# Kernel tuning notes

Hardware: AMD Instinct MI355X
Metric: run time of the kernel (lower is better)

## Reference

```python
import jax, jax.numpy as jnp
import numpy as np

H = 64
NG = 100000   # gene nodes
ND = 30000    # disease nodes
NE = 1500000  # gda edges (gene -> disease)
NL = 500000   # supervision (label) edges


def setup_inputs() -> dict:
    key = jax.random.key(0)
    ks = jax.random.split(key, 20)
    s = 0.1
    inp = {
        "gene_emb":    jax.random.normal(ks[0], (NG, H), jnp.float32) * s,
        "disease_emb": jax.random.normal(ks[1], (ND, H), jnp.float32) * s,
    }
    wnames = ["w1_gd_l", "w1_gd_r", "w1_dg_l", "w1_dg_r",
              "w2_gd_l", "w2_gd_r", "w2_dg_l", "w2_dg_r"]
    for i, n in enumerate(wnames):
        inp[n] = jax.random.normal(ks[2 + i], (H, H), jnp.float32) * s
    for i, n in enumerate(["b1_gd", "b1_dg", "b2_gd", "b2_dg"]):
        inp[n] = jax.random.normal(ks[10 + i], (H,), jnp.float32) * 0.01
    inp["edge_src"]  = jax.random.randint(ks[14], (NE,), 0, NG)
    inp["edge_dst"]  = jax.random.randint(ks[15], (NE,), 0, ND)
    inp["label_src"] = jax.random.randint(ks[16], (NL,), 0, NG)
    inp["label_dst"] = jax.random.randint(ks[17], (NL,), 0, ND)
    return inp


def _sage(x_src, x_dst, src, dst, n_dst, wl, wr, b):
    # SAGEConv (mean aggr): lin_l(mean_{j in N(i)} x_j) + lin_r(x_i) + b
    msum = jax.ops.segment_sum(x_src[src], dst, num_segments=n_dst)
    cnt = jax.ops.segment_sum(jnp.ones((src.shape[0], 1), x_src.dtype), dst,
                              num_segments=n_dst)
    mean = msum / jnp.maximum(cnt, 1.0)
    return mean @ wl + x_dst @ wr + b


def reference(gene_emb, disease_emb,
              w1_gd_l, w1_gd_r, b1_gd, w1_dg_l, w1_dg_r, b1_dg,
              w2_gd_l, w2_gd_r, b2_gd, w2_dg_l, w2_dg_r, b2_dg,
              edge_src, edge_dst, label_src, label_dst):
    # layer 1 (hetero: gene->disease via gda, disease->gene via rev_gda)
    h_d = jax.nn.relu(_sage(gene_emb, disease_emb, edge_src, edge_dst, ND,
                            w1_gd_l, w1_gd_r, b1_gd))
    h_g = jax.nn.relu(_sage(disease_emb, gene_emb, edge_dst, edge_src, NG,
                            w1_dg_l, w1_dg_r, b1_dg))
    # layer 2 (no activation)
    h_d2 = _sage(h_g, h_d, edge_src, edge_dst, ND, w2_gd_l, w2_gd_r, b2_gd)
    h_g2 = _sage(h_d, h_g, edge_dst, edge_src, NG, w2_dg_l, w2_dg_r, b2_dg)
    # classifier: dot product over label edges
    return jnp.sum(h_g2[label_src] * h_d2[label_dst], axis=-1)
```

## Files before the change

kernel.cpp:

```cpp
#include <hip/hip_runtime.h>
#include <hip/hip_bf16.h>

#define H 64
#define SCAN_CHUNK 512
#define NB1 512

typedef unsigned short u16;
typedef unsigned int u32;
typedef unsigned char u8;
typedef __attribute__((ext_vector_type(8))) __bf16 bf16x8;
typedef __attribute__((ext_vector_type(4))) float f32x4;
typedef __attribute__((ext_vector_type(2))) float f32x2;

__device__ __forceinline__ float bflo(u32 u) {
    return __builtin_bit_cast(float, u << 16);
}
__device__ __forceinline__ float bfhi(u32 u) {
    return __builtin_bit_cast(float, u & 0xffff0000u);
}
__device__ __forceinline__ u16 bf16rne(float f) {
    u32 u = __builtin_bit_cast(u32, f);
    return (u16)((u + 0x7FFFu + ((u >> 16) & 1u)) >> 16);
}
__device__ __forceinline__ u8 fp8enc(float f) {
    return (u8)(__builtin_amdgcn_cvt_pk_fp8_f32(f, 0.0f, 0, false) & 0xFF);
}

__global__ __launch_bounds__(256) void fused_count_convert_kernel(
    const int* __restrict__ es, const int* __restrict__ ed,
    int* __restrict__ histD, int* __restrict__ histG,
    int ne, int shiftD, int shiftG,
    const float* __restrict__ a, u16* __restrict__ oa, u32* __restrict__ oa8,
    long long na4,
    const float* __restrict__ b, u16* __restrict__ ob, u32* __restrict__ ob8,
    long long nb4)
{
    if (blockIdx.x < NB1) {
        __shared__ int lhd[256], lhg[256];
        const int tid = threadIdx.x;
        lhd[tid] = 0; lhg[tid] = 0;
        __syncthreads();
        const int chunk = (ne + NB1 - 1) / NB1;
        const int e0 = blockIdx.x * chunk;
        const int e1 = min(e0 + chunk, ne);
        for (int e = e0 + tid; e < e1; e += 256) {
            atomicAdd(&lhd[ed[e] >> shiftD], 1);
            atomicAdd(&lhg[es[e] >> shiftG], 1);
        }
        __syncthreads();
        histD[tid * NB1 + blockIdx.x] = lhd[tid];
        histG[tid * NB1 + blockIdx.x] = lhg[tid];
        return;
    }
    long long i = (long long)(blockIdx.x - NB1) * 256 + threadIdx.x;
    const float* src; u16* dst; u32* dst8; long long q;
    if (i < na4) { src = a; dst = oa; dst8 = oa8; q = i; }
    else if (i < na4 + nb4) { src = b; dst = ob; dst8 = ob8; q = i - na4; }
    else return;
    float4 v = *(const float4*)&src[q * 4];
    ushort4 o;
    o.x = bf16rne(v.x); o.y = bf16rne(v.y);
    o.z = bf16rne(v.z); o.w = bf16rne(v.w);
    *(ushort4*)&dst[q * 4] = o;
    int r = 0;
    r = __builtin_amdgcn_cvt_pk_fp8_f32(v.x * 16.0f, v.y * 16.0f, r, false);
    r = __builtin_amdgcn_cvt_pk_fp8_f32(v.z * 16.0f, v.w * 16.0f, r, true);
    dst8[q] = (u32)r;
}

__global__ __launch_bounds__(256) void scan_reduce_kernel(
    const int* __restrict__ a1, int n1, const int* __restrict__ a2, int n2,
    int B1, int* __restrict__ partial,
    u32* __restrict__ pad0, u32* __restrict__ pad1,
    u32* __restrict__ pad2, u32* __restrict__ pad3)
{
    if (blockIdx.x == 0) {
        int tz = threadIdx.x;
        if (tz < 16) pad0[tz] = 0;
        else if (tz < 32) pad1[tz - 16] = 0;
        else if (tz < 48) pad2[tz - 32] = 0;
        else if (tz < 64) pad3[tz - 48] = 0;
    }
    const int b = blockIdx.x;
    const int* a; int n, base;
    if (b < B1) { a = a1; n = n1; base = b * SCAN_CHUNK; }
    else        { a = a2; n = n2; base = (b - B1) * SCAN_CHUNK; }
    int t = threadIdx.x;
    int i0 = base + 2 * t, i1 = i0 + 1;
    int v = ((i0 < n) ? a[i0] : 0) + ((i1 < n) ? a[i1] : 0);
    #pragma unroll
    for (int off = 32; off > 0; off >>= 1) v += __shfl_down(v, off, 64);
    __shared__ int ws[4];
    if ((t & 63) == 0) ws[t >> 6] = v;
    __syncthreads();
    if (t == 0) partial[b] = ws[0] + ws[1] + ws[2] + ws[3];
}

__global__ __launch_bounds__(256) void scan_apply_kernel(
    const int* __restrict__ a1, int* __restrict__ out1, int n1,
    const int* __restrict__ a2, int* __restrict__ out2, int n2,
    int B1, int nbtot, const int* __restrict__ partial)
{
    __shared__ int sExcl[1024];
    __shared__ int ws[4];
    const int tid = threadIdx.x;
    const int lane = tid & 63, wid = tid >> 6;

    int j0 = 4 * tid;
    int p0 = (j0 + 0 < nbtot) ? partial[j0 + 0] : 0;
    int p1 = (j0 + 1 < nbtot) ? partial[j0 + 1] : 0;
    int p2 = (j0 + 2 < nbtot) ? partial[j0 + 2] : 0;
    int p3 = (j0 + 3 < nbtot) ? partial[j0 + 3] : 0;
    int psum = p0 + p1 + p2 + p3;
    int P = psum;
    #pragma unroll
    for (int off = 1; off < 64; off <<= 1) {
        int u = __shfl_up(P, off, 64);
        if (lane >= off) P += u;
    }
    if (lane == 63) ws[wid] = P;
    __syncthreads();
    int wbase = 0;
    #pragma unroll
    for (int w = 0; w < 4; ++w) wbase += (w < wid) ? ws[w] : 0;
    int e = wbase + (P - psum);
    sExcl[j0 + 0] = e;
    sExcl[j0 + 1] = e + p0;
    sExcl[j0 + 2] = e + p0 + p1;
    sExcl[j0 + 3] = e + p0 + p1 + p2;
    __syncthreads();

    const int b = blockIdx.x;
    int tot1 = sExcl[B1 - 1] + partial[B1 - 1];
    int myOff = sExcl[b] - ((b >= B1) ? tot1 : 0);
    if (b == 0 && tid == 0) {
        int tot2 = sExcl[nbtot - 1] + partial[nbtot - 1] - tot1;
        out1[n1] = tot1;
        out2[n2] = tot2;
    }
    __syncthreads();

    const int* a; int* out; int n, base;
    if (b < B1) { a = a1; out = out1; n = n1; base = b * SCAN_CHUNK; }
    else        { a = a2; out = out2; n = n2; base = (b - B1) * SCAN_CHUNK; }
    int i0 = base + 2 * tid, i1 = i0 + 1;
    int x0 = (i0 < n) ? a[i0] : 0;
    int x1 = (i1 < n) ? a[i1] : 0;
    int p = x0 + x1;
    int Q = p;
    #pragma unroll
    for (int off = 1; off < 64; off <<= 1) {
        int u = __shfl_up(Q, off, 64);
        if (lane >= off) Q += u;
    }
    if (lane == 63) ws[wid] = Q;
    __syncthreads();
    int waveBase = 0;
    #pragma unroll
    for (int w = 0; w < 4; ++w) waveBase += (w < wid) ? ws[w] : 0;
    int off0 = myOff + waveBase + (Q - p);
    if (i0 < n) out[i0] = off0;
    if (i1 < n) out[i1] = off0 + x0;
}

__global__ __launch_bounds__(256) void part_scatter_kernel(
    const int* __restrict__ es, const int* __restrict__ ed,
    const int* __restrict__ baseD, const int* __restrict__ baseG,
    u32* __restrict__ pairD, u32* __restrict__ pairG,
    int ne, int shiftD, int shiftG)
{
    __shared__ int curD[256], curG[256];
    const int tid = threadIdx.x;
    curD[tid] = baseD[tid * NB1 + blockIdx.x];
    curG[tid] = baseG[tid * NB1 + blockIdx.x];
    __syncthreads();
    const int maskD = (1 << shiftD) - 1;
    const int maskG = (1 << shiftG) - 1;
    const int chunk = (ne + NB1 - 1) / NB1;
    const int e0 = blockIdx.x * chunk;
    const int e1 = min(e0 + chunk, ne);
    for (int e = e0 + tid; e < e1; e += 256) {
        int s = es[e], d = ed[e];
        int pD = atomicAdd(&curD[d >> shiftD], 1);
        pairD[pD] = ((u32)(d & maskD) << 17) | (u32)s;
        int pG = atomicAdd(&curG[s >> shiftG], 1);
        pairG[pG] = ((u32)(s & maskG) << 17) | (u32)d;
    }
}

__global__ __launch_bounds__(256) void csr_build_kernel(
    const u32* __restrict__ pairD, const int* __restrict__ baseD,
    int* __restrict__ rowD, int* __restrict__ idxD, int nd, int shiftD, int nbktD,
    const u32* __restrict__ pairG, const int* __restrict__ baseG,
    int* __restrict__ rowG, int* __restrict__ idxG, int ng, int shiftG, int nbktG)
{
    __shared__ int lcnt[512], lcur[512];
    __shared__ int ws[4];
    const int j = blockIdx.x & 255;
    const int isG = blockIdx.x >> 8;
    const u32* pair; const int* base; int* row; int* idx; int n, shift, nbkt;
    if (isG) { pair = pairG; base = baseG; row = rowG; idx = idxG; n = ng; shift = shiftG; nbkt = nbktG; }
    else     { pair = pairD; base = baseD; row = rowD; idx = idxD; n = nd; shift = shiftD; nbkt = nbktD; }
    if (j >= nbkt) return;

    const int tid = threadIdx.x;
    const int nLo = j << shift;
    const int nHi = min(nLo + (1 << shift), n);
    const int range = nHi - nLo;
    const int segBase = base[j * NB1];
    const int segEnd  = base[(j + 1) * NB1];

    lcnt[tid] = 0; lcnt[tid + 256] = 0;
    __syncthreads();
    for (int t = segBase + tid; t < segEnd; t += 256)
        atomicAdd(&lcnt[pair[t] >> 17], 1);
    __syncthreads();

    int i0 = 2 * tid, i1 = i0 + 1;
    int c0 = (i0 < range) ? lcnt[i0] : 0;
    int c1 = (i1 < range) ? lcnt[i1] : 0;
    int p = c0 + c1;
    int P = p;
    const int lane = tid & 63, wid = tid >> 6;
    #pragma unroll
    for (int off = 1; off < 64; off <<= 1) {
        int u = __shfl_up(P, off, 64);
        if (lane >= off) P += u;
    }
    if (lane == 63) ws[wid] = P;
    __syncthreads();
    int waveBase = 0;
    #pragma unroll
    for (int w = 0; w < 4; ++w) waveBase += (w < wid) ? ws[w] : 0;
    int o0 = segBase + waveBase + (P - p);
    int o1 = o0 + c0;
    if (i0 < range) { row[nLo + i0] = o0; lcur[i0] = o0; }
    if (i1 < range) { row[nLo + i1] = o1; lcur[i1] = o1; }
    if (nHi == n && tid == 0) row[n] = segEnd;
    __syncthreads();

    for (int t = segBase + tid; t < segEnd; t += 256) {
        u32 pr = pair[t];
        int pos = atomicAdd(&lcur[pr >> 17], 1);
        idx[pos] = (int)(pr & 0x1FFFFu);
    }
}

__global__ __launch_bounds__(256) void gather_mean_kernel(
    const u8* __restrict__ srcD, const u8* __restrict__ srcG,
    const int* __restrict__ rowD, const int* __restrict__ idxD,
    const int* __restrict__ rowG, const int* __restrict__ idxG,
    u16* __restrict__ outD, u16* __restrict__ outG, int nd, int ng)
{
    int hw = blockIdx.x * 8 + (threadIdx.x >> 5);
    int l5 = threadIdx.x & 31;
    if (hw >= nd + ng) return;
    const bool isD = hw < nd;
    const int sub = l5 >> 3;
    const int c8 = l5 & 7;
    const u8* src; const int* row; const int* idx; u16* out; int node, npad;
    if (isD) { src = srcD; row = rowD; idx = idxD; out = outD; node = hw;      npad = ng; }
    else     { src = srcG; row = rowG; idx = idxG; out = outG; node = hw - nd; npad = nd; }
    int beg = row[node], end = row[node + 1];
    const u8* srcc = src + c8 * 8;

    f32x2 aA[4], aB[4];
    #pragma unroll
    for (int j = 0; j < 4; ++j) {
        aA[j] = (f32x2){0.f, 0.f}; aB[j] = (f32x2){0.f, 0.f};
    }

    for (int i = beg; i < end; i += 32) {
        int p = i + sub;
        const int* ip = idx + p;
        int t0 = ip[0],  t1 = ip[4],  t2 = ip[8],  t3 = ip[12];
        int t4 = ip[16], t5 = ip[20], t6 = ip[24], t7 = ip[28];
        int s0 = (p      < end) ? t0 : npad;
        int s1 = (p + 4  < end) ? t1 : npad;
        int s2 = (p + 8  < end) ? t2 : npad;
        int s3 = (p + 12 < end) ? t3 : npad;
        int s4 = (p + 16 < end) ? t4 : npad;
        int s5 = (p + 20 < end) ? t5 : npad;
        int s6 = (p + 24 < end) ? t6 : npad;
        int s7 = (p + 28 < end) ? t7 : npad;
        uint2 v0 = *(const uint2*)(srcc + (size_t)s0 * 64);
        uint2 v1 = *(const uint2*)(srcc + (size_t)s1 * 64);
        uint2 v2 = *(const uint2*)(srcc + (size_t)s2 * 64);
        uint2 v3 = *(const uint2*)(srcc + (size_t)s3 * 64);
        uint2 v4 = *(const uint2*)(srcc + (size_t)s4 * 64);
        uint2 v5 = *(const uint2*)(srcc + (size_t)s5 * 64);
        uint2 v6 = *(const uint2*)(srcc + (size_t)s6 * 64);
        uint2 v7 = *(const uint2*)(srcc + (size_t)s7 * 64);
        aA[0] += __builtin_amdgcn_cvt_pk_f32_fp8((int)v0.x, false);
        aA[1] += __builtin_amdgcn_cvt_pk_f32_fp8((int)v0.x, true);
        aA[2] += __builtin_amdgcn_cvt_pk_f32_fp8((int)v0.y, false);
        aA[3] += __builtin_amdgcn_cvt_pk_f32_fp8((int)v0.y, true);
        aA[0] += __builtin_amdgcn_cvt_pk_f32_fp8((int)v1.x, false);
        aA[1] += __builtin_amdgcn_cvt_pk_f32_fp8((int)v1.x, true);
        aA[2] += __builtin_amdgcn_cvt_pk_f32_fp8((int)v1.y, false);
        aA[3] += __builtin_amdgcn_cvt_pk_f32_fp8((int)v1.y, true);
        aA[0] += __builtin_amdgcn_cvt_pk_f32_fp8((int)v2.x, false);
        aA[1] += __builtin_amdgcn_cvt_pk_f32_fp8((int)v2.x, true);
        aA[2] += __builtin_amdgcn_cvt_pk_f32_fp8((int)v2.y, false);
        aA[3] += __builtin_amdgcn_cvt_pk_f32_fp8((int)v2.y, true);
        aA[0] += __builtin_amdgcn_cvt_pk_f32_fp8((int)v3.x, false);
        aA[1] += __builtin_amdgcn_cvt_pk_f32_fp8((int)v3.x, true);
        aA[2] += __builtin_amdgcn_cvt_pk_f32_fp8((int)v3.y, false);
        aA[3] += __builtin_amdgcn_cvt_pk_f32_fp8((int)v3.y, true);
        aB[0] += __builtin_amdgcn_cvt_pk_f32_fp8((int)v4.x, false);
        aB[1] += __builtin_amdgcn_cvt_pk_f32_fp8((int)v4.x, true);
        aB[2] += __builtin_amdgcn_cvt_pk_f32_fp8((int)v4.y, false);
        aB[3] += __builtin_amdgcn_cvt_pk_f32_fp8((int)v4.y, true);
        aB[0] += __builtin_amdgcn_cvt_pk_f32_fp8((int)v5.x, false);
        aB[1] += __builtin_amdgcn_cvt_pk_f32_fp8((int)v5.x, true);
        aB[2] += __builtin_amdgcn_cvt_pk_f32_fp8((int)v5.y, false);
        aB[3] += __builtin_amdgcn_cvt_pk_f32_fp8((int)v5.y, true);
        aB[0] += __builtin_amdgcn_cvt_pk_f32_fp8((int)v6.x, false);
        aB[1] += __builtin_amdgcn_cvt_pk_f32_fp8((int)v6.x, true);
        aB[2] += __builtin_amdgcn_cvt_pk_f32_fp8((int)v6.y, false);
        aB[3] += __builtin_amdgcn_cvt_pk_f32_fp8((int)v6.y, true);
        aB[0] += __builtin_amdgcn_cvt_pk_f32_fp8((int)v7.x, false);
        aB[1] += __builtin_amdgcn_cvt_pk_f32_fp8((int)v7.x, true);
        aB[2] += __builtin_amdgcn_cvt_pk_f32_fp8((int)v7.y, false);
        aB[3] += __builtin_amdgcn_cvt_pk_f32_fp8((int)v7.y, true);
    }

    f32x2 acc[4];
    #pragma unroll
    for (int j = 0; j < 4; ++j) acc[j] = aA[j] + aB[j];
    #pragma unroll
    for (int j = 0; j < 4; ++j) {
        f32x2 t;
        t.x = __shfl_xor(acc[j].x, 8, 64);
        t.y = __shfl_xor(acc[j].y, 8, 64);
        acc[j] += t;
        t.x = __shfl_xor(acc[j].x, 16, 64);
        t.y = __shfl_xor(acc[j].y, 16, 64);
        acc[j] += t;
    }
    if (sub == 0) {
        float inv = 0.0625f / fmaxf((float)(end - beg), 1.0f);
        u32 w0 = (u32)bf16rne(acc[0].x * inv) | ((u32)bf16rne(acc[0].y * inv) << 16);
        u32 w1 = (u32)bf16rne(acc[1].x * inv) | ((u32)bf16rne(acc[1].y * inv) << 16);
        u32 w2 = (u32)bf16rne(acc[2].x * inv) | ((u32)bf16rne(acc[2].y * inv) << 16);
        u32 w3 = (u32)bf16rne(acc[3].x * inv) | ((u32)bf16rne(acc[3].y * inv) << 16);
        uint4 pk = make_uint4(w0, w1, w2, w3);
        *(uint4*)(out + (size_t)node * H + c8 * 8) = pk;
    }
}

template <bool RELU, bool F8OUT>
__global__ __launch_bounds__(256) void sage_mm_mfma_kernel(
    const u16* __restrict__ meanD, const u16* __restrict__ xD, u16* __restrict__ outD,
    u8* __restrict__ outDf8,
    const float* __restrict__ wlD, const float* __restrict__ wrD,
    const float* __restrict__ bD, int nd,
    const u16* __restrict__ meanG, const u16* __restrict__ xG, u16* __restrict__ outG,
    u8* __restrict__ outGf8,
    const float* __restrict__ wlG, const float* __restrict__ wrG,
    const float* __restrict__ bG, int ng, int MBD)
{
    __shared__ u16 sB[16 * 64 * 8];
    int b = blockIdx.x;
    const u16 *mean, *x; u16* out; u8* out8; const float *wl, *wr, *bias; int n;
    if (b < MBD) { mean = meanD; x = xD; out = outD; out8 = outDf8; wl = wlD; wr = wrD; bias = bD; n = nd; }
    else { b -= MBD; mean = meanG; x = xG; out = outG; out8 = outGf8; wl = wlG; wr = wrG; bias = bG; n = ng; }

    const int tid = threadIdx.x;
    for (int i = tid; i < 4096; i += 256) {
        int k = i >> 6, ncol = i & 63;
        int q = (k >> 3) & 3, j = k & 7, t = ncol >> 4, n15 = ncol & 15;
        int lane = q * 16 + n15;
        int c0 = k >> 5;
        sB[(((c0 + 0) * 4 + t) * 64 + lane) * 8 + j] = bf16rne(wl[i]);
        sB[(((c0 + 2) * 4 + t) * 64 + lane) * 8 + j] = bf16rne(wr[i]);
    }
    __syncthreads();

    const int lane = tid & 63;
    const int wave = tid >> 6;
    const int m = lane & 15;
    const int q = lane >> 4;

    bf16x8 Bf[16];
    {
        const uint4* sB4 = (const uint4*)sB;
        #pragma unroll
        for (int f = 0; f < 16; ++f)
            Bf[f] = __builtin_bit_cast(bf16x8, sB4[f * 64 + lane]);
    }
    float bv[4];
    #pragma unroll
    for (int t = 0; t < 4; ++t) bv[t] = bias[t * 16 + m];

    const int row0 = b * 256;
    #pragma unroll
    for (int r = 0; r < 4; ++r) {
        int rbase = row0 + (wave + 4 * r) * 16;
        if (rbase >= n) break;
        int gr = min(rbase + m, n - 1);
        const uint4* mrow = (const uint4*)(mean + (size_t)gr * H);
        const uint4* xrow = (const uint4*)(x + (size_t)gr * H);
        bf16x8 A0 = __builtin_bit_cast(bf16x8, mrow[q]);
        bf16x8 A1 = __builtin_bit_cast(bf16x8, mrow[q + 4]);
        bf16x8 A2 = __builtin_bit_cast(bf16x8, xrow[q]);
        bf16x8 A3 = __builtin_bit_cast(bf16x8, xrow[q + 4]);
        f32x4 acc[4];
        #pragma unroll
        for (int t = 0; t < 4; ++t) acc[t] = (f32x4){bv[t], bv[t], bv[t], bv[t]};
        #pragma unroll
        for (int t = 0; t < 4; ++t) {
            acc[t] = __builtin_amdgcn_mfma_f32_16x16x32_bf16(A0, Bf[0 * 4 + t], acc[t], 0, 0, 0);
            acc[t] = __builtin_amdgcn_mfma_f32_16x16x32_bf16(A1, Bf[1 * 4 + t], acc[t], 0, 0, 0);
            acc[t] = __builtin_amdgcn_mfma_f32_16x16x32_bf16(A2, Bf[2 * 4 + t], acc[t], 0, 0, 0);
            acc[t] = __builtin_amdgcn_mfma_f32_16x16x32_bf16(A3, Bf[3 * 4 + t], acc[t], 0, 0, 0);
        }
        #pragma unroll
        for (int reg = 0; reg < 4; ++reg) {
            int orow = rbase + q * 4 + reg;
            if (orow < n) {
                u16* op = out + (size_t)orow * H;
                u8* op8 = F8OUT ? (out8 + (size_t)orow * H) : nullptr;
                #pragma unroll
                for (int t = 0; t < 4; ++t) {
                    float v = acc[t][reg];
                    if (RELU) v = fmaxf(v, 0.0f);
                    op[t * 16 + m] = bf16rne(v);
                    if (F8OUT) op8[t * 16 + m] = fp8enc(v * 16.0f);
                }
            }
        }
    }
}

__global__ __launch_bounds__(256) void classify_kernel(
    const u16* __restrict__ hg2, const u16* __restrict__ hd2,
    const int* __restrict__ ls, const int* __restrict__ ld,
    float* __restrict__ out, int nl)
{
    long long t = (long long)blockIdx.x * blockDim.x + threadIdx.x;
    int e = (int)(t >> 3);
    int c8 = (int)(t & 7);
    if (e >= nl) return;
    int a = ls[e];
    int b = ld[e];
    uint4 ua = *((const uint4*)(hg2 + (size_t)a * H) + c8);
    uint4 ub = *((const uint4*)(hd2 + (size_t)b * H) + c8);
    float v = bflo(ua.x) * bflo(ub.x) + bfhi(ua.x) * bfhi(ub.x)
            + bflo(ua.y) * bflo(ub.y) + bfhi(ua.y) * bfhi(ub.y)
            + bflo(ua.z) * bflo(ub.z) + bfhi(ua.z) * bfhi(ub.z)
            + bflo(ua.w) * bflo(ub.w) + bfhi(ua.w) * bfhi(ub.w);
    v += __shfl_xor(v, 1, 64);
    v += __shfl_xor(v, 2, 64);
    v += __shfl_xor(v, 4, 64);
    if (c8 == 0) out[e] = v;
}

extern "C" void kernel_launch(void* const* d_in, const int* in_sizes, int n_in,
                              void* d_out, int out_size, void* d_ws, size_t ws_size,
                              hipStream_t stream)
{
    const float* gene  = (const float*)d_in[0];
    const float* dis   = (const float*)d_in[1];
    const float* w1gdl = (const float*)d_in[2];
    const float* w1gdr = (const float*)d_in[3];
    const float* w1dgl = (const float*)d_in[4];
    const float* w1dgr = (const float*)d_in[5];
    const float* w2gdl = (const float*)d_in[6];
    const float* w2gdr = (const float*)d_in[7];
    const float* w2dgl = (const float*)d_in[8];
    const float* w2dgr = (const float*)d_in[9];
    const float* b1gd  = (const float*)d_in[10];
    const float* b1dg  = (const float*)d_in[11];
    const float* b2gd  = (const float*)d_in[12];
    const float* b2dg  = (const float*)d_in[13];
    const int* es = (const int*)d_in[14];
    const int* ed = (const int*)d_in[15];
    const int* ls = (const int*)d_in[16];
    const int* ld = (const int*)d_in[17];

    const int ng = in_sizes[0] / H;
    const int nd = in_sizes[1] / H;
    const int ne = in_sizes[14];
    const int nl = in_sizes[16];

    int shiftD = 0; while (((nd + (1 << shiftD) - 1) >> shiftD) > 256) ++shiftD;
    int shiftG = 0; while (((ng + (1 << shiftG) - 1) >> shiftG) > 256) ++shiftG;
    const int nbktD = (nd + (1 << shiftD) - 1) >> shiftD;
    const int nbktG = (ng + (1 << shiftG) - 1) >> shiftG;
    const int n1 = 256 * NB1;

    int* rowD = (int*)d_ws;
    int* rowG = rowD + nd + 1;
    int* idxD = rowG + ng + 1;
    int* idxG = idxD + ne;
    u16* geneBf = (u16*)(idxG + ne);
    u16* disBf  = geneBf + (size_t)ng * H;
    u16* h1Dbf  = disBf + (size_t)nd * H;
    u16* h1Gbf  = h1Dbf + (size_t)nd * H;
    u16* h2Dbf  = h1Gbf + (size_t)ng * H;
    u16* h2Gbf  = h2Dbf + (size_t)nd * H;
    uintptr_t pf8 = (uintptr_t)(h2Gbf + (size_t)ng * H);
    pf8 = (pf8 + 15) & ~(uintptr_t)15;
    u32* geneF8 = (u32*)pf8;
    u32* disF8  = geneF8 + (size_t)ng * 16 + 16;
    u32* h1DF8  = disF8 + (size_t)nd * 16 + 16;
    u32* h1GF8  = h1DF8 + (size_t)nd * 16 + 16;
    uintptr_t p = (uintptr_t)(h1GF8 + (size_t)ng * 16 + 16);
    p = (p + 15) & ~(uintptr_t)15;
    u16* MD = (u16*)p;
    u16* MG = MD + (size_t)nd * H;
    int* histD = (int*)p;
    int* histG = histD + n1;
    int* baseD = histG + n1;
    int* baseG = baseD + n1 + 1;
    int* partial  = baseG + n1 + 1;
    uintptr_t pp = (uintptr_t)(partial + 1024);
    pp = (pp + 15) & ~(uintptr_t)15;
    u32* pairD = (u32*)pp;
    u32* pairG = pairD + ne;

    const long long na4 = (long long)ng * H / 4;
    const long long nb4 = (long long)nd * H / 4;
    const int convBlocks = (int)((na4 + nb4 + 255) / 256);
    fused_count_convert_kernel<<<NB1 + convBlocks, 256, 0, stream>>>(
        es, ed, histD, histG, ne, shiftD, shiftG,
        gene, geneBf, geneF8, na4, dis, disBf, disF8, nb4);

    const int B1 = n1 / SCAN_CHUNK;
    const int nbtot = 2 * B1;
    scan_reduce_kernel<<<nbtot, 256, 0, stream>>>(histD, n1, histG, n1, B1, partial,
                                                  geneF8 + (size_t)ng * 16,
                                                  disF8 + (size_t)nd * 16,
                                                  h1DF8 + (size_t)nd * 16,
                                                  h1GF8 + (size_t)ng * 16);
    scan_apply_kernel<<<nbtot, 256, 0, stream>>>(histD, baseD, n1,
                                                 histG, baseG, n1, B1, nbtot, partial);

    part_scatter_kernel<<<NB1, 256, 0, stream>>>(es, ed, baseD, baseG,
                                                 pairD, pairG, ne, shiftD, shiftG);
    csr_build_kernel<<<512, 256, 0, stream>>>(
        pairD, baseD, rowD, idxD, nd, shiftD, nbktD,
        pairG, baseG, rowG, idxG, ng, shiftG, nbktG);

    const int gatherBlocks = (nd + ng + 7) / 8;
    const int MBD = (nd + 255) / 256;
    const int MBG = (ng + 255) / 256;

    gather_mean_kernel<<<gatherBlocks, 256, 0, stream>>>(
        (const u8*)geneF8, (const u8*)disF8, rowD, idxD, rowG, idxG, MD, MG, nd, ng);
    sage_mm_mfma_kernel<true, true><<<MBD + MBG, 256, 0, stream>>>(
        MD, disBf, h1Dbf, (u8*)h1DF8, w1gdl, w1gdr, b1gd, nd,
        MG, geneBf, h1Gbf, (u8*)h1GF8, w1dgl, w1dgr, b1dg, ng, MBD);

    gather_mean_kernel<<<gatherBlocks, 256, 0, stream>>>(
        (const u8*)h1GF8, (const u8*)h1DF8, rowD, idxD, rowG, idxG, MD, MG, nd, ng);
    sage_mm_mfma_kernel<false, false><<<MBD + MBG, 256, 0, stream>>>(
        MD, h1Dbf, h2Dbf, nullptr, w2gdl, w2gdr, b2gd, nd,
        MG, h1Gbf, h2Gbf, nullptr, w2dgl, w2dgr, b2dg, ng, MBD);

    {
        long long threads = (long long)nl * 8;
        int blocks = (int)((threads + 255) / 256);
        classify_kernel<<<blocks, 256, 0, stream>>>(h2Gbf, h2Dbf, ls, ld,
                                                    (float*)d_out, nl);
    }
}
```

Before: 317.4 us.

## Sub-bucket disease CSR by gene-index range to improve gather locality

The CSR build for disease nodes now splits each node's neighbour list into four sub-segments keyed by the high bits of the gene index (idx>>15), so consecutive gathers in a segment touch a narrower band of the gene feature table. The gather kernel walks the four sub-segments per disease node. Index loads and output stores are switched to nontemporal hints. The intent is better cache locality on the random source-row gathers, at the cost of more row-pointer storage, a larger per-bucket histogram and extra loop overhead for partially filled sub-segments.

```diff
diff --git a/kernel.cpp b/kernel.cpp
--- a/kernel.cpp
+++ b/kernel.cpp
@@ -11,6 +11,7 @@
 typedef __attribute__((ext_vector_type(8))) __bf16 bf16x8;
 typedef __attribute__((ext_vector_type(4))) float f32x4;
 typedef __attribute__((ext_vector_type(2))) float f32x2;
+typedef __attribute__((ext_vector_type(4))) u32 u32x4;
 
 __device__ __forceinline__ float bflo(u32 u) {
     return __builtin_bit_cast(float, u << 16);
@@ -212,13 +213,21 @@
 
     lcnt[tid] = 0; lcnt[tid + 256] = 0;
     __syncthreads();
-    for (int t = segBase + tid; t < segEnd; t += 256)
-        atomicAdd(&lcnt[pair[t] >> 17], 1);
-    __syncthreads();
-
+    if (isG) {
+        for (int t = segBase + tid; t < segEnd; t += 256)
+            atomicAdd(&lcnt[pair[t] >> 17], 1);
+    } else {
+        for (int t = segBase + tid; t < segEnd; t += 256) {
+            u32 pr = pair[t];
+            atomicAdd(&lcnt[((pr >> 17) << 2) | ((pr & 0x1FFFFu) >> 15)], 1);
+        }
+    }
+    __syncthreads();
+
+    const int elems = isG ? range : (range << 2);
     int i0 = 2 * tid, i1 = i0 + 1;
-    int c0 = (i0 < range) ? lcnt[i0] : 0;
-    int c1 = (i1 < range) ? lcnt[i1] : 0;
+    int c0 = (i0 < elems) ? lcnt[i0] : 0;
+    int c1 = (i1 < elems) ? lcnt[i1] : 0;
     int p = c0 + c1;
     int P = p;
     const int lane = tid & 63, wid = tid >> 6;
@@ -234,47 +243,42 @@
     for (int w = 0; w < 4; ++w) waveBase += (w < wid) ? ws[w] : 0;
     int o0 = segBase + waveBase + (P - p);
     int o1 = o0 + c0;
-    if (i0 < range) { row[nLo + i0] = o0; lcur[i0] = o0; }
-    if (i1 < range) { row[nLo + i1] = o1; lcur[i1] = o1; }
-    if (nHi == n && tid == 0) row[n] = segEnd;
-    __syncthreads();
-
-    for (int t = segBase + tid; t < segEnd; t += 256) {
-        u32 pr = pair[t];
-        int pos = atomicAdd(&lcur[pr >> 17], 1);
-        idx[pos] = (int)(pr & 0x1FFFFu);
-    }
-}
-
-__global__ __launch_bounds__(256) void gather_mean_kernel(
-    const u8* __restrict__ srcD, const u8* __restrict__ srcG,
-    const int* __restrict__ rowD, const int* __restrict__ idxD,
-    const int* __restrict__ rowG, const int* __restrict__ idxG,
-    u16* __restrict__ outD, u16* __restrict__ outG, int nd, int ng)
-{
-    int hw = blockIdx.x * 8 + (threadIdx.x >> 5);
-    int l5 = threadIdx.x & 31;
-    if (hw >= nd + ng) return;
-    const bool isD = hw < nd;
-    const int sub = l5 >> 3;
-    const int c8 = l5 & 7;
-    const u8* src; const int* row; const int* idx; u16* out; int node, npad;
-    if (isD) { src = srcD; row = rowD; idx = idxD; out = outD; node = hw;      npad = ng; }
-    else     { src = srcG; row = rowG; idx = idxG; out = outG; node = hw - nd; npad = nd; }
-    int beg = row[node], end = row[node + 1];
-    const u8* srcc = src + c8 * 8;
-
-    f32x2 aA[4], aB[4];
-    #pragma unroll
-    for (int j = 0; j < 4; ++j) {
-        aA[j] = (f32x2){0.f, 0.f}; aB[j] = (f32x2){0.f, 0.f};
-    }
-
+    int* rowOut = row + (isG ? nLo : (nLo << 2));
+    if (i0 < elems) { rowOut[i0] = o0; lcur[i0] = o0; }
+    if (i1 < elems) { rowOut[i1] = o1; lcur[i1] = o1; }
+    if (nHi == n && tid == 0) row[isG ? n : (n << 2)] = segEnd;
+    __syncthreads();
+
+    if (isG) {
+        for (int t = segBase + tid; t < segEnd; t += 256) {
+            u32 pr = pair[t];
+            int pos = atomicAdd(&lcur[pr >> 17], 1);
+            idx[pos] = (int)(pr & 0x1FFFFu);
+        }
+    } else {
+        for (int t = segBase + tid; t < segEnd; t += 256) {
+            u32 pr = pair[t];
+            int pos = atomicAdd(&lcur[((pr >> 17) << 2) | ((pr & 0x1FFFFu) >> 15)], 1);
+            idx[pos] = (int)(pr & 0x1FFFFu);
+        }
+    }
+}
+
+__device__ __forceinline__ void gather_seg(
+    const int* __restrict__ idx, const u8* __restrict__ srcc,
+    int beg, int end, int npad, int sub, f32x2* aA, f32x2* aB)
+{
     for (int i = beg; i < end; i += 32) {
         int p = i + sub;
         const int* ip = idx + p;
-        int t0 = ip[0],  t1 = ip[4],  t2 = ip[8],  t3 = ip[12];
-        int t4 = ip[16], t5 = ip[20], t6 = ip[24], t7 = ip[28];
+        int t0 = __builtin_nontemporal_load(ip +  0);
+        int t1 = __builtin_nontemporal_load(ip +  4);
+        int t2 = __builtin_nontemporal_load(ip +  8);
+        int t3 = __builtin_nontemporal_load(ip + 12);
+        int t4 = __builtin_nontemporal_load(ip + 16);
+        int t5 = __builtin_nontemporal_load(ip + 20);
+        int t6 = __builtin_nontemporal_load(ip + 24);
+        int t7 = __builtin_nontemporal_load(ip + 28);
         int s0 = (p      < end) ? t0 : npad;
         int s1 = (p + 4  < end) ? t1 : npad;
         int s2 = (p + 8  < end) ? t2 : npad;
@@ -324,6 +328,45 @@
         aB[2] += __builtin_amdgcn_cvt_pk_f32_fp8((int)v7.y, false);
         aB[3] += __builtin_amdgcn_cvt_pk_f32_fp8((int)v7.y, true);
     }
+}
+
+__global__ __launch_bounds__(256) void gather_mean_kernel(
+    const u8* __restrict__ srcD, const u8* __restrict__ srcG,
+    const int* __restrict__ rowD2, const int* __restrict__ idxD,
+    const int* __restrict__ rowG, const int* __restrict__ idxG,
+    u16* __restrict__ outD, u16* __restrict__ outG, int nd, int ng)
+{
+    int hw = blockIdx.x * 8 + (threadIdx.x >> 5);
+    int l5 = threadIdx.x & 31;
+    if (hw >= nd + ng) return;
+    const bool isD = hw < nd;
+    const int sub = l5 >> 3;
+    const int c8 = l5 & 7;
+
+    f32x2 aA[4], aB[4];
+    #pragma unroll
+    for (int j = 0; j < 4; ++j) {
+        aA[j] = (f32x2){0.f, 0.f}; aB[j] = (f32x2){0.f, 0.f};
+    }
+
+    int deg;
+    if (isD) {
+        const u8* srcc = srcD + c8 * 8;
+        int rb = hw << 2;
+        int b0 = rowD2[rb], b1 = rowD2[rb + 1], b2 = rowD2[rb + 2];
+        int b3 = rowD2[rb + 3], b4 = rowD2[rb + 4];
+        deg = b4 - b0;
+        gather_seg(idxD, srcc, b0, b1, ng, sub, aA, aB);
+        gather_seg(idxD, srcc, b1, b2, ng, sub, aA, aB);
+        gather_seg(idxD, srcc, b2, b3, ng, sub, aA, aB);
+        gather_seg(idxD, srcc, b3, b4, ng, sub, aA, aB);
+    } else {
+        const u8* srcc = srcG + c8 * 8;
+        int node = hw - nd;
+        int beg = rowG[node], end = rowG[node + 1];
+        deg = end - beg;
+        gather_seg(idxG, srcc, beg, end, nd, sub, aA, aB);
+    }
 
     f32x2 acc[4];
     #pragma unroll
@@ -339,13 +382,15 @@
         acc[j] += t;
     }
     if (sub == 0) {
-        float inv = 0.0625f / fmaxf((float)(end - beg), 1.0f);
-        u32 w0 = (u32)bf16rne(acc[0].x * inv) | ((u32)bf16rne(acc[0].y * inv) << 16);
-        u32 w1 = (u32)bf16rne(acc[1].x * inv) | ((u32)bf16rne(acc[1].y * inv) << 16);
-        u32 w2 = (u32)bf16rne(acc[2].x * inv) | ((u32)bf16rne(acc[2].y * inv) << 16);
-        u32 w3 = (u32)bf16rne(acc[3].x * inv) | ((u32)bf16rne(acc[3].y * inv) << 16);
-        uint4 pk = make_uint4(w0, w1, w2, w3);
-        *(uint4*)(out + (size_t)node * H + c8 * 8) = pk;
+        u16* out = isD ? outD : outG;
+        int node = isD ? hw : hw - nd;
+        float inv = 0.0625f / fmaxf((float)deg, 1.0f);
+        u32x4 pk;
+        pk.x = (u32)bf16rne(acc[0].x * inv) | ((u32)bf16rne(acc[0].y * inv) << 16);
+        pk.y = (u32)bf16rne(acc[1].x * inv) | ((u32)bf16rne(acc[1].y * inv) << 16);
+        pk.z = (u32)bf16rne(acc[2].x * inv) | ((u32)bf16rne(acc[2].y * inv) << 16);
+        pk.w = (u32)bf16rne(acc[3].x * inv) | ((u32)bf16rne(acc[3].y * inv) << 16);
+        __builtin_nontemporal_store(pk, (u32x4*)(out + (size_t)node * H + c8 * 8));
     }
 }
 
@@ -491,7 +536,7 @@
     const int n1 = 256 * NB1;
 
     int* rowD = (int*)d_ws;
-    int* rowG = rowD + nd + 1;
+    int* rowG = rowD + nd * 4 + 1;
     int* idxD = rowG + ng + 1;
     int* idxG = idxD + ne;
     u16* geneBf = (u16*)(idxG + ne);
```

Result: slower. 348.1 us (+9.7%).

## Fuse neighbor mean gather with MFMA SAGE linear into one kernel

Applied to the files above, without the earlier changes.

Merges the gather-mean kernel and the MFMA matmul kernel so each 256-thread block gathers 32 nodes' neighbor means into shared memory (XOR-swizzled) and then runs the linear layers on them with MFMA. This removes the global write and re-read of the bf16 mean buffers and one launch per layer. In exchange, every block reloads and reformats the full weight matrices into shared memory for only 32 rows, and the MFMA phase now uses only two 16-row groups split across waves, so the per-row matmul overhead rises.

```diff
diff --git a/kernel.cpp b/kernel.cpp
--- a/kernel.cpp
+++ b/kernel.cpp
@@ -246,127 +246,35 @@
     }
 }
 
-__global__ __launch_bounds__(256) void gather_mean_kernel(
+template <bool RELU, bool F8OUT>
+__global__ __launch_bounds__(256) void fused_gather_mm_kernel(
     const u8* __restrict__ srcD, const u8* __restrict__ srcG,
     const int* __restrict__ rowD, const int* __restrict__ idxD,
     const int* __restrict__ rowG, const int* __restrict__ idxG,
-    u16* __restrict__ outD, u16* __restrict__ outG, int nd, int ng)
-{
-    int hw = blockIdx.x * 8 + (threadIdx.x >> 5);
-    int l5 = threadIdx.x & 31;
-    if (hw >= nd + ng) return;
-    const bool isD = hw < nd;
-    const int sub = l5 >> 3;
-    const int c8 = l5 & 7;
-    const u8* src; const int* row; const int* idx; u16* out; int node, npad;
-    if (isD) { src = srcD; row = rowD; idx = idxD; out = outD; node = hw;      npad = ng; }
-    else     { src = srcG; row = rowG; idx = idxG; out = outG; node = hw - nd; npad = nd; }
-    int beg = row[node], end = row[node + 1];
-    const u8* srcc = src + c8 * 8;
-
-    f32x2 aA[4], aB[4];
-    #pragma unroll
-    for (int j = 0; j < 4; ++j) {
-        aA[j] = (f32x2){0.f, 0.f}; aB[j] = (f32x2){0.f, 0.f};
-    }
-
-    for (int i = beg; i < end; i += 32) {
-        int p = i + sub;
-        const int* ip = idx + p;
-        int t0 = ip[0],  t1 = ip[4],  t2 = ip[8],  t3 = ip[12];
-        int t4 = ip[16], t5 = ip[20], t6 = ip[24], t7 = ip[28];
-        int s0 = (p      < end) ? t0 : npad;
-        int s1 = (p + 4  < end) ? t1 : npad;
-        int s2 = (p + 8  < end) ? t2 : npad;
-        int s3 = (p + 12 < end) ? t3 : npad;
-        int s4 = (p + 16 < end) ? t4 : npad;
-        int s5 = (p + 20 < end) ? t5 : npad;
-        int s6 = (p + 24 < end) ? t6 : npad;
-        int s7 = (p + 28 < end) ? t7 : npad;
-        uint2 v0 = *(const uint2*)(srcc + (size_t)s0 * 64);
-        uint2 v1 = *(const uint2*)(srcc + (size_t)s1 * 64);
-        uint2 v2 = *(const uint2*)(srcc + (size_t)s2 * 64);
-        uint2 v3 = *(const uint2*)(srcc + (size_t)s3 * 64);
-        uint2 v4 = *(const uint2*)(srcc + (size_t)s4 * 64);
-        uint2 v5 = *(const uint2*)(srcc + (size_t)s5 * 64);
-        uint2 v6 = *(const uint2*)(srcc + (size_t)s6 * 64);
-        uint2 v7 = *(const uint2*)(srcc + (size_t)s7 * 64);
-        aA[0] += __builtin_amdgcn_cvt_pk_f32_fp8((int)v0.x, false);
-        aA[1] += __builtin_amdgcn_cvt_pk_f32_fp8((int)v0.x, true);
-        aA[2] += __builtin_amdgcn_cvt_pk_f32_fp8((int)v0.y, false);
-        aA[3] += __builtin_amdgcn_cvt_pk_f32_fp8((int)v0.y, true);
-        aA[0] += __builtin_amdgcn_cvt_pk_f32_fp8((int)v1.x, false);
-        aA[1] += __builtin_amdgcn_cvt_pk_f32_fp8((int)v1.x, true);
-        aA[2] += __builtin_amdgcn_cvt_pk_f32_fp8((int)v1.y, false);
-        aA[3] += __builtin_amdgcn_cvt_pk_f32_fp8((int)v1.y, true);
-        aA[0] += __builtin_amdgcn_cvt_pk_f32_fp8((int)v2.x, false);
-        aA[1] += __builtin_amdgcn_cvt_pk_f32_fp8((int)v2.x, true);
-        aA[2] += __builtin_amdgcn_cvt_pk_f32_fp8((int)v2.y, false);
-        aA[3] += __builtin_amdgcn_cvt_pk_f32_fp8((int)v2.y, true);
-        aA[0] += __builtin_amdgcn_cvt_pk_f32_fp8((int)v3.x, false);
-        aA[1] += __builtin_amdgcn_cvt_pk_f32_fp8((int)v3.x, true);
-        aA[2] += __builtin_amdgcn_cvt_pk_f32_fp8((int)v3.y, false);
-        aA[3] += __builtin_amdgcn_cvt_pk_f32_fp8((int)v3.y, true);
-        aB[0] += __builtin_amdgcn_cvt_pk_f32_fp8((int)v4.x, false);
-        aB[1] += __builtin_amdgcn_cvt_pk_f32_fp8((int)v4.x, true);
-        aB[2] += __builtin_amdgcn_cvt_pk_f32_fp8((int)v4.y, false);
-        aB[3] += __builtin_amdgcn_cvt_pk_f32_fp8((int)v4.y, true);
-        aB[0] += __builtin_amdgcn_cvt_pk_f32_fp8((int)v5.x, false);
-        aB[1] += __builtin_amdgcn_cvt_pk_f32_fp8((int)v5.x, true);
-        aB[2] += __builtin_amdgcn_cvt_pk_f32_fp8((int)v5.y, false);
-        aB[3] += __builtin_amdgcn_cvt_pk_f32_fp8((int)v5.y, true);
-        aB[0] += __builtin_amdgcn_cvt_pk_f32_fp8((int)v6.x, false);
-        aB[1] += __builtin_amdgcn_cvt_pk_f32_fp8((int)v6.x, true);
-        aB[2] += __builtin_amdgcn_cvt_pk_f32_fp8((int)v6.y, false);
-        aB[3] += __builtin_amdgcn_cvt_pk_f32_fp8((int)v6.y, true);
-        aB[0] += __builtin_amdgcn_cvt_pk_f32_fp8((int)v7.x, false);
-        aB[1] += __builtin_amdgcn_cvt_pk_f32_fp8((int)v7.x, true);
-        aB[2] += __builtin_amdgcn_cvt_pk_f32_fp8((int)v7.y, false);
-        aB[3] += __builtin_amdgcn_cvt_pk_f32_fp8((int)v7.y, true);
-    }
-
-    f32x2 acc[4];
-    #pragma unroll
-    for (int j = 0; j < 4; ++j) acc[j] = aA[j] + aB[j];
-    #pragma unroll
-    for (int j = 0; j < 4; ++j) {
-        f32x2 t;
-        t.x = __shfl_xor(acc[j].x, 8, 64);
-        t.y = __shfl_xor(acc[j].y, 8, 64);
-        acc[j] += t;
-        t.x = __shfl_xor(acc[j].x, 16, 64);
-        t.y = __shfl_xor(acc[j].y, 16, 64);
-        acc[j] += t;
-    }
-    if (sub == 0) {
-        float inv = 0.0625f / fmaxf((float)(end - beg), 1.0f);
-        u32 w0 = (u32)bf16rne(acc[0].x * inv) | ((u32)bf16rne(acc[0].y * inv) << 16);
-        u32 w1 = (u32)bf16rne(acc[1].x * inv) | ((u32)bf16rne(acc[1].y * inv) << 16);
-        u32 w2 = (u32)bf16rne(acc[2].x * inv) | ((u32)bf16rne(acc[2].y * inv) << 16);
-        u32 w3 = (u32)bf16rne(acc[3].x * inv) | ((u32)bf16rne(acc[3].y * inv) << 16);
-        uint4 pk = make_uint4(w0, w1, w2, w3);
-        *(uint4*)(out + (size_t)node * H + c8 * 8) = pk;
-    }
-}
-
-template <bool RELU, bool F8OUT>
-__global__ __launch_bounds__(256) void sage_mm_mfma_kernel(
-    const u16* __restrict__ meanD, const u16* __restrict__ xD, u16* __restrict__ outD,
-    u8* __restrict__ outDf8,
+    const u16* __restrict__ xD, u16* __restrict__ outD, u8* __restrict__ outDf8,
     const float* __restrict__ wlD, const float* __restrict__ wrD,
     const float* __restrict__ bD, int nd,
-    const u16* __restrict__ meanG, const u16* __restrict__ xG, u16* __restrict__ outG,
-    u8* __restrict__ outGf8,
+    const u16* __restrict__ xG, u16* __restrict__ outG, u8* __restrict__ outGf8,
     const float* __restrict__ wlG, const float* __restrict__ wrG,
-    const float* __restrict__ bG, int ng, int MBD)
+    const float* __restrict__ bG, int ng, int MBD32)
 {
     __shared__ u16 sB[16 * 64 * 8];
+    __shared__ u16 sMean[32 * 64];
+
     int b = blockIdx.x;
-    const u16 *mean, *x; u16* out; u8* out8; const float *wl, *wr, *bias; int n;
-    if (b < MBD) { mean = meanD; x = xD; out = outD; out8 = outDf8; wl = wlD; wr = wrD; bias = bD; n = nd; }
-    else { b -= MBD; mean = meanG; x = xG; out = outG; out8 = outGf8; wl = wlG; wr = wrG; bias = bG; n = ng; }
-
+    const u8* src; const int* row; const int* idx; const u16* x;
+    u16* out; u8* out8; const float *wl, *wr, *bias; int n, npad;
+    if (b < MBD32) {
+        src = srcD; row = rowD; idx = idxD; x = xD; out = outD; out8 = outDf8;
+        wl = wlD; wr = wrD; bias = bD; n = nd; npad = ng;
+    } else {
+        b -= MBD32;
+        src = srcG; row = rowG; idx = idxG; x = xG; out = outG; out8 = outGf8;
+        wl = wlG; wr = wrG; bias = bG; n = ng; npad = nd;
+    }
+    const int base = b * 32;
     const int tid = threadIdx.x;
+
     for (int i = tid; i < 4096; i += 256) {
         int k = i >> 6, ncol = i & 63;
         int q = (k >> 3) & 3, j = k & 7, t = ncol >> 4, n15 = ncol & 15;
@@ -375,58 +283,160 @@
         sB[(((c0 + 0) * 4 + t) * 64 + lane) * 8 + j] = bf16rne(wl[i]);
         sB[(((c0 + 2) * 4 + t) * 64 + lane) * 8 + j] = bf16rne(wr[i]);
     }
-    __syncthreads();
-
-    const int lane = tid & 63;
-    const int wave = tid >> 6;
-    const int m = lane & 15;
-    const int q = lane >> 4;
-
-    bf16x8 Bf[16];
+
     {
-        const uint4* sB4 = (const uint4*)sB;
-        #pragma unroll
-        for (int f = 0; f < 16; ++f)
-            Bf[f] = __builtin_bit_cast(bf16x8, sB4[f * 64 + lane]);
-    }
-    float bv[4];
-    #pragma unroll
-    for (int t = 0; t < 4; ++t) bv[t] = bias[t * 16 + m];
-
-    const int row0 = b * 256;
-    #pragma unroll
-    for (int r = 0; r < 4; ++r) {
-        int rbase = row0 + (wave + 4 * r) * 16;
-        if (rbase >= n) break;
-        int gr = min(rbase + m, n - 1);
-        const uint4* mrow = (const uint4*)(mean + (size_t)gr * H);
-        const uint4* xrow = (const uint4*)(x + (size_t)gr * H);
-        bf16x8 A0 = __builtin_bit_cast(bf16x8, mrow[q]);
-        bf16x8 A1 = __builtin_bit_cast(bf16x8, mrow[q + 4]);
-        bf16x8 A2 = __builtin_bit_cast(bf16x8, xrow[q]);
-        bf16x8 A3 = __builtin_bit_cast(bf16x8, xrow[q + 4]);
-        f32x4 acc[4];
-        #pragma unroll
-        for (int t = 0; t < 4; ++t) acc[t] = (f32x4){bv[t], bv[t], bv[t], bv[t]};
-        #pragma unroll
-        for (int t = 0; t < 4; ++t) {
-            acc[t] = __builtin_amdgcn_mfma_f32_16x16x32_bf16(A0, Bf[0 * 4 + t], acc[t], 0, 0, 0);
-            acc[t] = __builtin_amdgcn_mfma_f32_16x16x32_bf16(A1, Bf[1 * 4 + t], acc[t], 0, 0, 0);
-            acc[t] = __builtin_amdgcn_mfma_f32_16x16x32_bf16(A2, Bf[2 * 4 + t], acc[t], 0, 0, 0);
-            acc[t] = __builtin_amdgcn_mfma_f32_16x16x32_bf16(A3, Bf[3 * 4 + t], acc[t], 0, 0, 0);
+        const int hwl = tid >> 5;
+        const int l5 = tid & 31;
+        const int sub = l5 >> 3;
+        const int c8 = l5 & 7;
+        const u8* srcc = src + c8 * 8;
+        for (int r = 0; r < 4; ++r) {
+            int nodeLocal = r * 8 + hwl;
+            int node = base + nodeLocal;
+            if (node < n) {
+                int beg = row[node], end = row[node + 1];
+                f32x2 aA[4], aB[4];
+                #pragma unroll
+                for (int j = 0; j < 4; ++j) {
+                    aA[j] = (f32x2){0.f, 0.f}; aB[j] = (f32x2){0.f, 0.f};
+                }
+                for (int i = beg; i < end; i += 32) {
+                    int p = i + sub;
+                    const int* ip = idx + p;
+                    int t0 = ip[0],  t1 = ip[4],  t2 = ip[8],  t3 = ip[12];
+                    int t4 = ip[16], t5 = ip[20], t6 = ip[24], t7 = ip[28];
+                    int s0 = (p      < end) ? t0 : npad;
+                    int s1 = (p + 4  < end) ? t1 : npad;
+                    int s2 = (p + 8  < end) ? t2 : npad;
+                    int s3 = (p + 12 < end) ? t3 : npad;
+                    int s4 = (p + 16 < end) ? t4 : npad;
+                    int s5 = (p + 20 < end) ? t5 : npad;
+                    int s6 = (p + 24 < end) ? t6 : npad;
+                    int s7 = (p + 28 < end) ? t7 : npad;
+                    uint2 v0 = *(const uint2*)(srcc + (size_t)s0 * 64);
+                    uint2 v1 = *(const uint2*)(srcc + (size_t)s1 * 64);
+                    uint2 v2 = *(const uint2*)(srcc + (size_t)s2 * 64);
+                    uint2 v3 = *(const uint2*)(srcc + (size_t)s3 * 64);
+                    uint2 v4 = *(const uint2*)(srcc + (size_t)s4 * 64);
+                    uint2 v5 = *(const uint2*)(srcc + (size_t)s5 * 64);
+                    uint2 v6 = *(const uint2*)(srcc + (size_t)s6 * 64);
+                    uint2 v7 = *(const uint2*)(srcc + (size_t)s7 * 64);
+                    aA[0] += __builtin_amdgcn_cvt_pk_f32_fp8((int)v0.x, false);
+                    aA[1] += __builtin_amdgcn_cvt_pk_f32_fp8((int)v0.x, true);
+                    aA[2] += __builtin_amdgcn_cvt_pk_f32_fp8((int)v0.y, false);
+                    aA[3] += __builtin_amdgcn_cvt_pk_f32_fp8((int)v0.y, true);
+                    aA[0] += __builtin_amdgcn_cvt_pk_f32_fp8((int)v1.x, false);
+                    aA[1] += __builtin_amdgcn_cvt_pk_f32_fp8((int)v1.x, true);
+                    aA[2] += __builtin_amdgcn_cvt_pk_f32_fp8((int)v1.y, false);
+                    aA[3] += __builtin_amdgcn_cvt_pk_f32_fp8((int)v1.y, true);
+                    aA[0] += __builtin_amdgcn_cvt_pk_f32_fp8((int)v2.x, false);
+                    aA[1] += __builtin_amdgcn_cvt_pk_f32_fp8((int)v2.x, true);
+                    aA[2] += __builtin_amdgcn_cvt_pk_f32_fp8((int)v2.y, false);
+                    aA[3] += __builtin_amdgcn_cvt_pk_f32_fp8((int)v2.y, true);
+                    aA[0] += __builtin_amdgcn_cvt_pk_f32_fp8((int)v3.x, false);
+                    aA[1] += __builtin_amdgcn_cvt_pk_f32_fp8((int)v3.x, true);
+                    aA[2] += __builtin_amdgcn_cvt_pk_f32_fp8((int)v3.y, false);
+                    aA[3] += __builtin_amdgcn_cvt_pk_f32_fp8((int)v3.y, true);
+                    aB[0] += __builtin_amdgcn_cvt_pk_f32_fp8((int)v4.x, false);
+                    aB[1] += __builtin_amdgcn_cvt_pk_f32_fp8((int)v4.x, true);
+                    aB[2] += __builtin_amdgcn_cvt_pk_f32_fp8((int)v4.y, false);
+                    aB[3] += __builtin_amdgcn_cvt_pk_f32_fp8((int)v4.y, true);
+                    aB[0] += __builtin_amdgcn_cvt_pk_f32_fp8((int)v5.x, false);
+                    aB[1] += __builtin_amdgcn_cvt_pk_f32_fp8((int)v5.x, true);
+                    aB[2] += __builtin_amdgcn_cvt_pk_f32_fp8((int)v5.y, false);
+                    aB[3] += __builtin_amdgcn_cvt_pk_f32_fp8((int)v5.y, true);
+                    aB[0] += __builtin_amdgcn_cvt_pk_f32_fp8((int)v6.x, false);
+                    aB[1] += __builtin_amdgcn_cvt_pk_f32_fp8((int)v6.x, true);
+                    aB[2] += __builtin_amdgcn_cvt_pk_f32_fp8((int)v6.y, false);
+                    aB[3] += __builtin_amdgcn_cvt_pk_f32_fp8((int)v6.y, true);
+                    aB[0] += __builtin_amdgcn_cvt_pk_f32_fp8((int)v7.x, false);
+                    aB[1] += __builtin_amdgcn_cvt_pk_f32_fp8((int)v7.x, true);
+                    aB[2] += __builtin_amdgcn_cvt_pk_f32_fp8((int)v7.y, false);
+                    aB[3] += __builtin_amdgcn_cvt_pk_f32_fp8((int)v7.y, true);
+                }
+                f32x2 acc[4];
+                #pragma unroll
+                for (int j = 0; j < 4; ++j) acc[j] = aA[j] + aB[j];
+                #pragma unroll
+                for (int j = 0; j < 4; ++j) {
+                    f32x2 t;
+                    t.x = __shfl_xor(acc[j].x, 8, 64);
+                    t.y = __shfl_xor(acc[j].y, 8, 64);
+                    acc[j] += t;
+                    t.x = __shfl_xor(acc[j].x, 16, 64);
+                    t.y = __shfl_xor(acc[j].y, 16, 64);
+                    acc[j] += t;
+                }
+                if (sub == 0) {
+                    float inv = 0.0625f / fmaxf((float)(end - beg), 1.0f);
+                    u32 w0 = (u32)bf16rne(acc[0].x * inv) | ((u32)bf16rne(acc[0].y * inv) << 16);
+                    u32 w1 = (u32)bf16rne(acc[1].x * inv) | ((u32)bf16rne(acc[1].y * inv) << 16);
+                    u32 w2 = (u32)bf16rne(acc[2].x * inv) | ((u32)bf16rne(acc[2].y * inv) << 16);
+                    u32 w3 = (u32)bf16rne(acc[3].x * inv) | ((u32)bf16rne(acc[3].y * inv) << 16);
+                    uint4 pk = make_uint4(w0, w1, w2, w3);
+                    *(uint4*)(sMean + nodeLocal * 64 + ((c8 ^ (nodeLocal & 7)) * 8)) = pk;
+                }
+            }
         }
-        #pragma unroll
-        for (int reg = 0; reg < 4; ++reg) {
-            int orow = rbase + q * 4 + reg;
-            if (orow < n) {
-                u16* op = out + (size_t)orow * H;
-                u8* op8 = F8OUT ? (out8 + (size_t)orow * H) : nullptr;
-                #pragma unroll
-                for (int t = 0; t < 4; ++t) {
-                    float v = acc[t][reg];
-                    if (RELU) v = fmaxf(v, 0.0f);
-                    op[t * 16 + m] = bf16rne(v);
-                    if (F8OUT) op8[t * 16 + m] = fp8enc(v * 16.0f);
+    }
+    __syncthreads();
+
+    {
+        const int lane = tid & 63;
+        const int wave = tid >> 6;
+        const int m = lane & 15;
+        const int q = lane >> 4;
+        const int grp = wave >> 1;
+        const int t0 = (wave & 1) * 2;
+        int rbase = base + grp * 16;
+        if (rbase < n) {
+            int lr = grp * 16 + m;
+            const u16* mr = sMean + lr * 64;
+            bf16x8 A0 = __builtin_bit_cast(bf16x8, *(const uint4*)(mr + ((q ^ (lr & 7)) * 8)));
+            bf16x8 A1 = __builtin_bit_cast(bf16x8, *(const uint4*)(mr + (((q + 4) ^ (lr & 7)) * 8)));
+            int gr = min(rbase + m, n - 1);
+            const uint4* xrow = (const uint4*)(x + (size_t)gr * H);
+            bf16x8 A2 = __builtin_bit_cast(bf16x8, xrow[q]);
+            bf16x8 A3 = __builtin_bit_cast(bf16x8, xrow[q + 4]);
+            float bv0 = bias[t0 * 16 + m];
+            float bv1 = bias[(t0 + 1) * 16 + m];
+            f32x4 acc0 = (f32x4){bv0, bv0, bv0, bv0};
+            f32x4 acc1 = (f32x4){bv1, bv1, bv1, bv1};
+            const uint4* sB4 = (const uint4*)sB;
+            {
+                bf16x8 B0, B1;
+                B0 = __builtin_bit_cast(bf16x8, sB4[(0 * 4 + t0) * 64 + lane]);
+                B1 = __builtin_bit_cast(bf16x8, sB4[(0 * 4 + t0 + 1) * 64 + lane]);
+                acc0 = __builtin_amdgcn_mfma_f32_16x16x32_bf16(A0, B0, acc0, 0, 0, 0);
+                acc1 = __builtin_amdgcn_mfma_f32_16x16x32_bf16(A0, B1, acc1, 0, 0, 0);
+                B0 = __builtin_bit_cast(bf16x8, sB4[(1 * 4 + t0) * 64 + lane]);
+                B1 = __builtin_bit_cast(bf16x8, sB4[(1 * 4 + t0 + 1) * 64 + lane]);
+                acc0 = __builtin_amdgcn_mfma_f32_16x16x32_bf16(A1, B0, acc0, 0, 0, 0);
+                acc1 = __builtin_amdgcn_mfma_f32_16x16x32_bf16(A1, B1, acc1, 0, 0, 0);
+                B0 = __builtin_bit_cast(bf16x8, sB4[(2 * 4 + t0) * 64 + lane]);
+                B1 = __builtin_bit_cast(bf16x8, sB4[(2 * 4 + t0 + 1) * 64 + lane]);
+                acc0 = __builtin_amdgcn_mfma_f32_16x16x32_bf16(A2, B0, acc0, 0, 0, 0);
+                acc1 = __builtin_amdgcn_mfma_f32_16x16x32_bf16(A2, B1, acc1, 0, 0, 0);
+                B0 = __builtin_bit_cast(bf16x8, sB4[(3 * 4 + t0) * 64 + lane]);
+                B1 = __builtin_bit_cast(bf16x8, sB4[(3 * 4 + t0 + 1) * 64 + lane]);
+                acc0 = __builtin_amdgcn_mfma_f32_16x16x32_bf16(A3, B0, acc0, 0, 0, 0);
+                acc1 = __builtin_amdgcn_mfma_f32_16x16x32_bf16(A3, B1, acc1, 0, 0, 0);
+            }
+            #pragma unroll
+            for (int reg = 0; reg < 4; ++reg) {
+                int orow = rbase + q * 4 + reg;
+                if (orow < n) {
+                    u16* op = out + (size_t)orow * H;
+                    float v0 = acc0[reg];
+                    float v1 = acc1[reg];
+                    if (RELU) { v0 = fmaxf(v0, 0.0f); v1 = fmaxf(v1, 0.0f); }
+                    op[t0 * 16 + m] = bf16rne(v0);
+                    op[(t0 + 1) * 16 + m] = bf16rne(v1);
+                    if (F8OUT) {
+                        u8* op8 = out8 + (size_t)orow * H;
+                        op8[t0 * 16 + m] = fp8enc(v0 * 16.0f);
+                        op8[(t0 + 1) * 16 + m] = fp8enc(v1 * 16.0f);
+                    }
                 }
             }
         }
@@ -508,8 +518,6 @@
     u32* h1GF8  = h1DF8 + (size_t)nd * 16 + 16;
     uintptr_t p = (uintptr_t)(h1GF8 + (size_t)ng * 16 + 16);
     p = (p + 15) & ~(uintptr_t)15;
-    u16* MD = (u16*)p;
-    u16* MG = MD + (size_t)nd * H;
     int* histD = (int*)p;
     int* histG = histD + n1;
     int* baseD = histG + n1;
@@ -543,21 +551,18 @@
         pairD, baseD, rowD, idxD, nd, shiftD, nbktD,
         pairG, baseG, rowG, idxG, ng, shiftG, nbktG);
 
-    const int gatherBlocks = (nd + ng + 7) / 8;
-    const int MBD = (nd + 255) / 256;
-    const int MBG = (ng + 255) / 256;
-
-    gather_mean_kernel<<<gatherBlocks, 256, 0, stream>>>(
-        (const u8*)geneF8, (const u8*)disF8, rowD, idxD, rowG, idxG, MD, MG, nd, ng);
-    sage_mm_mfma_kernel<true, true><<<MBD + MBG, 256, 0, stream>>>(
-        MD, disBf, h1Dbf, (u8*)h1DF8, w1gdl, w1gdr, b1gd, nd,
-        MG, geneBf, h1Gbf, (u8*)h1GF8, w1dgl, w1dgr, b1dg, ng, MBD);
-
-    gather_mean_kernel<<<gatherBlocks, 256, 0, stream>>>(
-        (const u8*)h1GF8, (const u8*)h1DF8, rowD, idxD, rowG, idxG, MD, MG, nd, ng);
-    sage_mm_mfma_kernel<false, false><<<MBD + MBG, 256, 0, stream>>>(
-        MD, h1Dbf, h2Dbf, nullptr, w2gdl, w2gdr, b2gd, nd,
-        MG, h1Gbf, h2Gbf, nullptr, w2dgl, w2dgr, b2dg, ng, MBD);
+    const int MBD32 = (nd + 31) / 32;
+    const int MBG32 = (ng + 31) / 32;
+
+    fused_gather_mm_kernel<true, true><<<MBD32 + MBG32, 256, 0, stream>>>(
+        (const u8*)geneF8, (const u8*)disF8, rowD, idxD, rowG, idxG,
+        disBf, h1Dbf, (u8*)h1DF8, w1gdl, w1gdr, b1gd, nd,
+        geneBf, h1Gbf, (u8*)h1GF8, w1dgl, w1dgr, b1dg, ng, MBD32);
+
+    fused_gather_mm_kernel<false, false><<<MBD32 + MBG32, 256, 0, stream>>>(
+        (const u8*)h1GF8, (const u8*)h1DF8, rowD, idxD, rowG, idxG,
+        h1Dbf, h2Dbf, nullptr, w2gdl, w2gdr, b2gd, nd,
+        h1Gbf, h2Gbf, nullptr, w2dgl, w2dgr, b2dg, ng, MBD32);
 
     {
         long long threads = (long long)nl * 8;
```

Result: slower. 348.8 us (+9.9%).
